# Optimization experiments

Measured on AMD Instinct MI355X. Metric: run time of the kernel, lower is better.

The kernel has to match this reference:

```python
import jax, jax.numpy as jnp
import numpy as np

B, N, C = 8, 4096, 768
H = 8            # num_heads (hardcoded in module)
D = C // H       # head_dim = 96


def setup_inputs() -> dict:
    key = jax.random.key(0)
    ks = jax.random.split(key, 10)
    s = 0.02
    return {
        "x_rgb": jax.random.normal(ks[0], (B, N, C), dtype=jnp.float32),
        "x_depth": jax.random.normal(ks[1], (B, N, C), dtype=jnp.float32),
        "W_qkv_rgb": jax.random.normal(ks[2], (3 * C, C), dtype=jnp.float32) * s,
        "b_qkv_rgb": jnp.zeros((3 * C,), dtype=jnp.float32),
        "W_qkv_depth": jax.random.normal(ks[3], (2 * C, C), dtype=jnp.float32) * s,
        "b_qkv_depth": jnp.zeros((2 * C,), dtype=jnp.float32),
        "W_out": jax.random.normal(ks[4], (C, C), dtype=jnp.float32) * s,
        "b_out": jnp.zeros((C,), dtype=jnp.float32),
        "adaptive_weights": jnp.ones((2,), dtype=jnp.float32),
    }


def reference(x_rgb, x_depth, W_qkv_rgb, b_qkv_rgb, W_qkv_depth, b_qkv_depth,
              W_out, b_out, adaptive_weights):
    scale = 1.0 / (D ** 0.5)
    # qkv projections (torch Linear: x @ W.T + b)
    qkv_rgb = (x_rgb @ W_qkv_rgb.T + b_qkv_rgb).reshape(B, N, 3, H, D)
    q_rgb, k_rgb, v_rgb = qkv_rgb[:, :, 0], qkv_rgb[:, :, 1], qkv_rgb[:, :, 2]
    kv_depth = (x_depth @ W_qkv_depth.T + b_qkv_depth).reshape(B, N, 2, H, D)
    k_depth, v_depth = kv_depth[:, :, 0], kv_depth[:, :, 1]

    # per-token attention across the head axis: scores are [B,N,H,H]
    attn_rgb = jax.nn.softmax(
        jnp.einsum('bnqd,bnkd->bnqk', q_rgb, k_depth) * scale, axis=-1)
    attn_depth = jax.nn.softmax(
        jnp.einsum('bnqd,bnkd->bnqk', q_rgb, k_rgb) * scale, axis=-1)

    # NOTE: faithful to original einsum with independent labels k and v:
    # sums over k (softmax -> 1) and over v independently.
    wv_rgb = jnp.einsum('bnqk,bnvd->bnqd', attn_rgb, v_depth)
    wv_depth = jnp.einsum('bnqk,bnvd->bnqd', attn_depth, v_rgb)

    w = jax.nn.sigmoid(adaptive_weights)
    x_fusion = (w[0] * wv_rgb + w[1] * wv_depth).reshape(B, N, C)
    x_fusion = x_fusion @ W_out.T + b_out
    return (x_rgb, x_fusion)
```

## Files before the change

kernel.cpp:

```cpp
#include <hip/hip_runtime.h>

typedef unsigned short u16;
typedef __attribute__((ext_vector_type(8))) short bf16x8;
typedef __attribute__((ext_vector_type(4))) float f32x4;

#define M_TOT 32768

__device__ __forceinline__ u16 f2b(float x) {
    union { float f; unsigned u; } c; c.f = x;
    unsigned r = c.u + 0x7fffu + ((c.u >> 16) & 1u);
    return (u16)(r >> 16);
}

__global__ void prep_b1(const float* __restrict__ Wr, const float* __restrict__ Wd,
                        const float* __restrict__ br, const float* __restrict__ bd,
                        const float* __restrict__ aw,
                        u16* __restrict__ B1, float* __restrict__ fb) {
    int id = blockIdx.x * 256 + threadIdx.x;
    if (id >= 96 * 1536) return;
    int d = id / 1536, k = id - d * 1536;
    float w0 = 1.f / (1.f + __expf(-aw[0]));
    float w1 = 1.f / (1.f + __expf(-aw[1]));
    float s = 0.f, v;
    if (k < 768) {
        for (int h = 0; h < 8; h++) s += Wr[(size_t)(1536 + h * 96 + d) * 768 + k];
        v = w1 * s;
    } else {
        for (int h = 0; h < 8; h++) s += Wd[(size_t)(768 + h * 96 + d) * 768 + (k - 768)];
        v = w0 * s;
    }
    B1[id] = f2b(v);
    if (k == 0) {
        float t = 0.f;
        for (int h = 0; h < 8; h++)
            t += w1 * br[1536 + h * 96 + d] + w0 * bd[768 + h * 96 + d];
        fb[d] = t;
    }
}

__global__ void prep_weff(const float* __restrict__ Wo, u16* __restrict__ Weff) {
    int id = blockIdx.x * 256 + threadIdx.x;
    if (id >= 768 * 96) return;
    int c = id / 96, d = id - c * 96;
    float s = 0.f;
    for (int h = 0; h < 8; h++) s += Wo[(size_t)c * 768 + h * 96 + d];
    Weff[id] = f2b(s);
}

#define LDF 72
__global__ __launch_bounds__(256) void gemm_f(const float* __restrict__ Xr,
                                              const float* __restrict__ Xd,
                                              const u16* __restrict__ B1,
                                              const float* __restrict__ fb,
                                              float* __restrict__ out0,
                                              u16* __restrict__ fbuf) {
    __shared__ u16 sA[64 * LDF];
    __shared__ u16 sB[96 * LDF];
    const int tid = threadIdx.x;
    const int m0 = blockIdx.x * 64;
    const int lane = tid & 63, wave = tid >> 6;
    const int fr = lane & 15, fk = (lane >> 4) * 8;

    f32x4 acc[6] = {};

    for (int ks = 0; ks < 24; ks++) {
        const int k0 = ks * 64;
        const float* __restrict__ X = (ks < 12) ? Xr : Xd;
        const int kx = (ks < 12) ? k0 : (k0 - 768);

#pragma unroll
        for (int r = 0; r < 4; r++) {
            int c = tid + 256 * r;
            int row = c >> 4, colc = (c & 15) * 4;
            float4 v = *(const float4*)&X[(size_t)(m0 + row) * 768 + kx + colc];
            if (ks < 12)
                *(float4*)&out0[(size_t)(m0 + row) * 768 + k0 + colc] = v;
            ushort4 bv;
            bv.x = f2b(v.x); bv.y = f2b(v.y); bv.z = f2b(v.z); bv.w = f2b(v.w);
            *(ushort4*)&sA[row * LDF + colc] = bv;
        }
#pragma unroll
        for (int r = 0; r < 3; r++) {
            int c = tid + 256 * r;
            int row = c >> 3, colc = (c & 7) * 8;
            *(uint4*)&sB[row * LDF + colc] =
                *(const uint4*)&B1[(size_t)row * 1536 + k0 + colc];
        }
        __syncthreads();

#pragma unroll
        for (int s = 0; s < 2; s++) {
            bf16x8 a = *(bf16x8*)&sA[(wave * 16 + fr) * LDF + s * 32 + fk];
#pragma unroll
            for (int j = 0; j < 6; j++) {
                bf16x8 b = *(bf16x8*)&sB[(j * 16 + fr) * LDF + s * 32 + fk];
                acc[j] = __builtin_amdgcn_mfma_f32_16x16x32_bf16(a, b, acc[j], 0, 0, 0);
            }
        }
        __syncthreads();
    }

    const int em = (lane >> 4) * 4, en = lane & 15;
#pragma unroll
    for (int j = 0; j < 6; j++) {
        int dcol = j * 16 + en;
        float bias = fb[dcol];
#pragma unroll
        for (int r = 0; r < 4; r++) {
            int row = m0 + wave * 16 + em + r;
            fbuf[(size_t)row * 96 + dcol] = f2b(acc[j][r] + bias);
        }
    }
}

#define LDO 104
__global__ __launch_bounds__(256) void gemm_o(const u16* __restrict__ fbuf,
                                              const u16* __restrict__ Weff,
                                              const float* __restrict__ bout,
                                              float* __restrict__ out1) {
    __shared__ u16 sA[128 * LDO];
    __shared__ u16 sB[128 * LDO];
    const int tid = threadIdx.x;
    const int n0 = blockIdx.x * 128, m0 = blockIdx.y * 128;

#pragma unroll
    for (int r = 0; r < 6; r++) {
        int c = tid + 256 * r;
        int row = c / 12, colc = (c - row * 12) * 8;
        *(uint4*)&sA[row * LDO + colc] =
            *(const uint4*)&fbuf[(size_t)(m0 + row) * 96 + colc];
        *(uint4*)&sB[row * LDO + colc] =
            *(const uint4*)&Weff[(size_t)(n0 + row) * 96 + colc];
    }
    __syncthreads();

    const int lane = tid & 63, wave = tid >> 6;
    const int wm = (wave >> 1) * 64, wn = (wave & 1) * 64;
    const int fr = lane & 15, fk = (lane >> 4) * 8;

    f32x4 acc[4][4] = {};
#pragma unroll
    for (int s = 0; s < 3; s++) {
        bf16x8 a[4], b[4];
#pragma unroll
        for (int i = 0; i < 4; i++)
            a[i] = *(bf16x8*)&sA[(wm + i * 16 + fr) * LDO + s * 32 + fk];
#pragma unroll
        for (int j = 0; j < 4; j++)
            b[j] = *(bf16x8*)&sB[(wn + j * 16 + fr) * LDO + s * 32 + fk];
#pragma unroll
        for (int i = 0; i < 4; i++)
#pragma unroll
            for (int j = 0; j < 4; j++)
                acc[i][j] = __builtin_amdgcn_mfma_f32_16x16x32_bf16(a[i], b[j], acc[i][j], 0, 0, 0);
    }

    const int em = (lane >> 4) * 4, en = lane & 15;
#pragma unroll
    for (int j = 0; j < 4; j++) {
        int col = n0 + wn + j * 16 + en;
        float bias = bout[col];
#pragma unroll
        for (int i = 0; i < 4; i++) {
#pragma unroll
            for (int r = 0; r < 4; r++) {
                out1[(size_t)(m0 + wm + i * 16 + em + r) * 768 + col] = acc[i][j][r] + bias;
            }
        }
    }
}

extern "C" void kernel_launch(void* const* d_in, const int* in_sizes, int n_in,
                              void* d_out, int out_size, void* d_ws, size_t ws_size,
                              hipStream_t stream) {
    const float* x_rgb       = (const float*)d_in[0];
    const float* x_depth     = (const float*)d_in[1];
    const float* W_qkv_rgb   = (const float*)d_in[2];
    const float* b_qkv_rgb   = (const float*)d_in[3];
    const float* W_qkv_depth = (const float*)d_in[4];
    const float* b_qkv_depth = (const float*)d_in[5];
    const float* W_out       = (const float*)d_in[6];
    const float* b_out       = (const float*)d_in[7];
    const float* aw          = (const float*)d_in[8];

    float* out0 = (float*)d_out;
    float* out1 = out0 + (size_t)M_TOT * 768;

    char* w = (char*)d_ws;
    u16*   B1   = (u16*)w;
    float* fb   = (float*)(w + 294912);
    u16*   Weff = (u16*)(w + 294912 + 512);
    u16*   fbuf = (u16*)(w + 294912 + 512 + 147456);

    prep_b1<<<576, 256, 0, stream>>>(W_qkv_rgb, W_qkv_depth, b_qkv_rgb, b_qkv_depth,
                                     aw, B1, fb);
    prep_weff<<<288, 256, 0, stream>>>(W_out, Weff);
    gemm_f<<<512, 256, 0, stream>>>(x_rgb, x_depth, B1, fb, out0, fbuf);
    gemm_o<<<dim3(6, 256), 256, 0, stream>>>(fbuf, Weff, b_out, out1);
}
```

Baseline: 407.9 us.

## Drop shared-memory staging in both GEMMs, load MFMA fragments straight from global

Both GEMM kernels stop staging tiles in LDS. Each wave now loads its A fragments directly from global memory, converting fp32 rows to bf16 in registers, and reads B fragments from the small L2-resident weight matrices. gemm_o is retiled so each block covers 16 rows and all 768 columns, and the out0 copy and out1 stores use nontemporal stores. This removes the LDS round-trips and barriers in a memory-bound pipeline, at the cost of less coalesced per-lane global loads and redundant B reads across waves.

```diff
diff --git a/kernel.cpp b/kernel.cpp
--- a/kernel.cpp
+++ b/kernel.cpp
@@ -10,6 +10,13 @@
     union { float f; unsigned u; } c; c.f = x;
     unsigned r = c.u + 0x7fffu + ((c.u >> 16) & 1u);
     return (u16)(r >> 16);
+}
+
+__device__ __forceinline__ bf16x8 cvt8(f32x4 a, f32x4 b) {
+    union { bf16x8 v; u16 s[8]; } r;
+    r.s[0] = f2b(a.x); r.s[1] = f2b(a.y); r.s[2] = f2b(a.z); r.s[3] = f2b(a.w);
+    r.s[4] = f2b(b.x); r.s[5] = f2b(b.y); r.s[6] = f2b(b.z); r.s[7] = f2b(b.w);
+    return r.v;
 }
 
 __global__ void prep_b1(const float* __restrict__ Wr, const float* __restrict__ Wd,
@@ -47,57 +54,54 @@
     Weff[id] = f2b(s);
 }
 
-#define LDF 72
 __global__ __launch_bounds__(256) void gemm_f(const float* __restrict__ Xr,
                                               const float* __restrict__ Xd,
                                               const u16* __restrict__ B1,
                                               const float* __restrict__ fb,
                                               float* __restrict__ out0,
                                               u16* __restrict__ fbuf) {
-    __shared__ u16 sA[64 * LDF];
-    __shared__ u16 sB[96 * LDF];
     const int tid = threadIdx.x;
-    const int m0 = blockIdx.x * 64;
     const int lane = tid & 63, wave = tid >> 6;
     const int fr = lane & 15, fk = (lane >> 4) * 8;
+    const int mrow = blockIdx.x * 64 + wave * 16;
+    const int m = mrow + fr;
+    const float* __restrict__ xr_row = Xr + (size_t)m * 768;
+    const float* __restrict__ xd_row = Xd + (size_t)m * 768;
+    float* __restrict__ o0_row = out0 + (size_t)m * 768;
 
     f32x4 acc[6] = {};
 
-    for (int ks = 0; ks < 24; ks++) {
-        const int k0 = ks * 64;
-        const float* __restrict__ X = (ks < 12) ? Xr : Xd;
-        const int kx = (ks < 12) ? k0 : (k0 - 768);
-
-#pragma unroll
-        for (int r = 0; r < 4; r++) {
-            int c = tid + 256 * r;
-            int row = c >> 4, colc = (c & 15) * 4;
-            float4 v = *(const float4*)&X[(size_t)(m0 + row) * 768 + kx + colc];
-            if (ks < 12)
-                *(float4*)&out0[(size_t)(m0 + row) * 768 + k0 + colc] = v;
-            ushort4 bv;
-            bv.x = f2b(v.x); bv.y = f2b(v.y); bv.z = f2b(v.z); bv.w = f2b(v.w);
-            *(ushort4*)&sA[row * LDF + colc] = bv;
-        }
-#pragma unroll
-        for (int r = 0; r < 3; r++) {
-            int c = tid + 256 * r;
-            int row = c >> 3, colc = (c & 7) * 8;
-            *(uint4*)&sB[row * LDF + colc] =
-                *(const uint4*)&B1[(size_t)row * 1536 + k0 + colc];
-        }
-        __syncthreads();
-
+#pragma unroll 2
+    for (int ks = 0; ks < 12; ks++) {
 #pragma unroll
         for (int s = 0; s < 2; s++) {
-            bf16x8 a = *(bf16x8*)&sA[(wave * 16 + fr) * LDF + s * 32 + fk];
+            const int kc = ks * 64 + s * 32 + fk;
+            f32x4 v0 = *(const f32x4*)&xr_row[kc];
+            f32x4 v1 = *(const f32x4*)&xr_row[kc + 4];
+            __builtin_nontemporal_store(v0, (f32x4*)&o0_row[kc]);
+            __builtin_nontemporal_store(v1, (f32x4*)&o0_row[kc + 4]);
+            bf16x8 a = cvt8(v0, v1);
 #pragma unroll
             for (int j = 0; j < 6; j++) {
-                bf16x8 b = *(bf16x8*)&sB[(j * 16 + fr) * LDF + s * 32 + fk];
+                bf16x8 b = *(const bf16x8*)&B1[(size_t)(j * 16 + fr) * 1536 + kc];
                 acc[j] = __builtin_amdgcn_mfma_f32_16x16x32_bf16(a, b, acc[j], 0, 0, 0);
             }
         }
-        __syncthreads();
+    }
+#pragma unroll 2
+    for (int ks = 0; ks < 12; ks++) {
+#pragma unroll
+        for (int s = 0; s < 2; s++) {
+            const int kc = ks * 64 + s * 32 + fk;
+            f32x4 v0 = *(const f32x4*)&xd_row[kc];
+            f32x4 v1 = *(const f32x4*)&xd_row[kc + 4];
+            bf16x8 a = cvt8(v0, v1);
+#pragma unroll
+            for (int j = 0; j < 6; j++) {
+                bf16x8 b = *(const bf16x8*)&B1[(size_t)(j * 16 + fr) * 1536 + 768 + kc];
+                acc[j] = __builtin_amdgcn_mfma_f32_16x16x32_bf16(a, b, acc[j], 0, 0, 0);
+            }
+        }
     }
 
     const int em = (lane >> 4) * 4, en = lane & 15;
@@ -106,67 +110,42 @@
         int dcol = j * 16 + en;
         float bias = fb[dcol];
 #pragma unroll
-        for (int r = 0; r < 4; r++) {
-            int row = m0 + wave * 16 + em + r;
-            fbuf[(size_t)row * 96 + dcol] = f2b(acc[j][r] + bias);
-        }
+        for (int r = 0; r < 4; r++)
+            fbuf[(size_t)(mrow + em + r) * 96 + dcol] = f2b(acc[j][r] + bias);
     }
 }
 
-#define LDO 104
 __global__ __launch_bounds__(256) void gemm_o(const u16* __restrict__ fbuf,
                                               const u16* __restrict__ Weff,
                                               const float* __restrict__ bout,
                                               float* __restrict__ out1) {
-    __shared__ u16 sA[128 * LDO];
-    __shared__ u16 sB[128 * LDO];
     const int tid = threadIdx.x;
-    const int n0 = blockIdx.x * 128, m0 = blockIdx.y * 128;
+    const int lane = tid & 63, wave = tid >> 6;
+    const int fr = lane & 15, fk = (lane >> 4) * 8;
+    const int m0 = blockIdx.x * 16;
+    const int nbase = wave * 192;
+    const u16* __restrict__ arow = fbuf + (size_t)(m0 + fr) * 96;
 
-#pragma unroll
-    for (int r = 0; r < 6; r++) {
-        int c = tid + 256 * r;
-        int row = c / 12, colc = (c - row * 12) * 8;
-        *(uint4*)&sA[row * LDO + colc] =
-            *(const uint4*)&fbuf[(size_t)(m0 + row) * 96 + colc];
-        *(uint4*)&sB[row * LDO + colc] =
-            *(const uint4*)&Weff[(size_t)(n0 + row) * 96 + colc];
-    }
-    __syncthreads();
-
-    const int lane = tid & 63, wave = tid >> 6;
-    const int wm = (wave >> 1) * 64, wn = (wave & 1) * 64;
-    const int fr = lane & 15, fk = (lane >> 4) * 8;
-
-    f32x4 acc[4][4] = {};
+    f32x4 acc[12] = {};
 #pragma unroll
     for (int s = 0; s < 3; s++) {
-        bf16x8 a[4], b[4];
+        bf16x8 a = *(const bf16x8*)&arow[s * 32 + fk];
 #pragma unroll
-        for (int i = 0; i < 4; i++)
-            a[i] = *(bf16x8*)&sA[(wm + i * 16 + fr) * LDO + s * 32 + fk];
-#pragma unroll
-        for (int j = 0; j < 4; j++)
-            b[j] = *(bf16x8*)&sB[(wn + j * 16 + fr) * LDO + s * 32 + fk];
-#pragma unroll
-        for (int i = 0; i < 4; i++)
-#pragma unroll
-            for (int j = 0; j < 4; j++)
-                acc[i][j] = __builtin_amdgcn_mfma_f32_16x16x32_bf16(a[i], b[j], acc[i][j], 0, 0, 0);
+        for (int j = 0; j < 12; j++) {
+            bf16x8 b = *(const bf16x8*)&Weff[(size_t)(nbase + j * 16 + fr) * 96 + s * 32 + fk];
+            acc[j] = __builtin_amdgcn_mfma_f32_16x16x32_bf16(a, b, acc[j], 0, 0, 0);
+        }
     }
 
     const int em = (lane >> 4) * 4, en = lane & 15;
 #pragma unroll
-    for (int j = 0; j < 4; j++) {
-        int col = n0 + wn + j * 16 + en;
+    for (int j = 0; j < 12; j++) {
+        int col = nbase + j * 16 + en;
         float bias = bout[col];
 #pragma unroll
-        for (int i = 0; i < 4; i++) {
-#pragma unroll
-            for (int r = 0; r < 4; r++) {
-                out1[(size_t)(m0 + wm + i * 16 + em + r) * 768 + col] = acc[i][j][r] + bias;
-            }
-        }
+        for (int r = 0; r < 4; r++)
+            __builtin_nontemporal_store(acc[j][r] + bias,
+                                        &out1[(size_t)(m0 + em + r) * 768 + col]);
     }
 }
 
@@ -196,5 +175,5 @@
                                      aw, B1, fb);
     prep_weff<<<288, 256, 0, stream>>>(W_out, Weff);
     gemm_f<<<512, 256, 0, stream>>>(x_rgb, x_depth, B1, fb, out0, fbuf);
-    gemm_o<<<dim3(6, 256), 256, 0, stream>>>(fbuf, Weff, b_out, out1);
+    gemm_o<<<2048, 256, 0, stream>>>(fbuf, Weff, b_out, out1);
 }
```

New measurement: 481.6 us. 18.1% more time.
